# Performance work log

Hardware: AMD Instinct MI355X
Metric: run time of the kernel (lower is better)

The kernel has to match this reference:

```python
import jax, jax.numpy as jnp
import numpy as np

PAD = 1
K = 3  # kernel_size


def conv2d(x, w, b):
    y = jax.lax.conv_general_dilated(
        x, w, window_strides=(1, 1), padding=((PAD, PAD), (PAD, PAD)),
        dimension_numbers=("NCHW", "OIHW", "NCHW"))
    return y + b[None, :, None, None]


def deform_conv2d(x, offset, weight, bias):
    # torchvision.ops.deform_conv2d semantics (stride=1, dilation=1, 1 offset group)
    B, C, H, W = x.shape
    O = weight.shape[0]
    K2 = K * K
    off = offset.reshape(B, K2, 2, H, W)  # [...,0]=dy, [...,1]=dx
    ky, kx = jnp.meshgrid(jnp.arange(K), jnp.arange(K), indexing="ij")
    ky = ky.reshape(K2).astype(x.dtype)
    kx = kx.reshape(K2).astype(x.dtype)
    hh = jnp.arange(H, dtype=x.dtype)
    ww = jnp.arange(W, dtype=x.dtype)
    # sampling coords, shape [B, K2, H, W]
    py = off[:, :, 0] + ky[None, :, None, None] + hh[None, None, :, None] - PAD
    px = off[:, :, 1] + kx[None, :, None, None] + ww[None, None, None, :] - PAD

    y0 = jnp.floor(py)
    x0 = jnp.floor(px)
    wy = (py - y0)[:, None]  # [B,1,K2,H,W]
    wx = (px - x0)[:, None]

    xf = x.reshape(B, C, H * W)

    def gather(iy, ix):
        valid = (iy >= 0) & (iy < H) & (ix >= 0) & (ix < W)
        iyc = jnp.clip(iy, 0, H - 1).astype(jnp.int32)
        ixc = jnp.clip(ix, 0, W - 1).astype(jnp.int32)
        idx = (iyc * W + ixc).reshape(B, 1, K2 * H * W)
        v = jnp.take_along_axis(xf, idx, axis=2).reshape(B, C, K2, H, W)
        return v * valid.reshape(B, 1, K2, H, W).astype(x.dtype)

    v00 = gather(y0, x0)
    v01 = gather(y0, x0 + 1)
    v10 = gather(y0 + 1, x0)
    v11 = gather(y0 + 1, x0 + 1)
    sampled = (v00 * (1 - wy) * (1 - wx) + v01 * (1 - wy) * wx
               + v10 * wy * (1 - wx) + v11 * wy * wx)  # [B,C,K2,H,W]
    out = jnp.einsum("bckhw,ock->bohw", sampled, weight.reshape(O, C, K2))
    return out + bias[None, :, None, None]


def setup_inputs() -> dict:
    key = jax.random.key(0)
    k1, k2, k3, k4, k5 = jax.random.split(key, 5)
    B, C, H, W = 4, 64, 192, 192
    O = 64
    x = jax.random.normal(k1, (B, C, H, W), dtype=jnp.float32)
    w_off = jax.random.normal(k2, (2 * K * K, C, K, K), dtype=jnp.float32) * 0.05
    b_off = jnp.zeros((2 * K * K,), dtype=jnp.float32)
    w_conv = jax.random.normal(k3, (O, C, K, K), dtype=jnp.float32) * (1.0 / np.sqrt(C * K * K))
    b_conv = jax.random.normal(k4, (O,), dtype=jnp.float32) * 0.01
    return {"x": x, "w_off": w_off, "b_off": b_off, "w_conv": w_conv, "b_conv": b_conv}


def reference(x, w_off, b_off, w_conv, b_conv):
    offset = conv2d(x, w_off, b_off)
    y = deform_conv2d(x, offset, w_conv, b_conv)
    return conv2d(y, w_conv, b_conv)  # module reuses self.conv on deform output
```

## Files before the change

### kernel.cpp

```cpp
#include <hip/hip_runtime.h>

constexpr int B = 4;
constexpr int C = 64;
constexpr int O = 64;
constexpr int OOFF = 18;
constexpr int H = 192;
constexpr int W = 192;

typedef __attribute__((ext_vector_type(8))) short short8;
typedef __attribute__((ext_vector_type(4))) float float4v;
typedef __attribute__((ext_vector_type(2))) float f32x2;
typedef __attribute__((ext_vector_type(2))) uint u32x2;
typedef __attribute__((ext_vector_type(2))) __bf16 bf16x2;

__device__ inline ushort f2bf(float f) {
  return __builtin_bit_cast(ushort, (__bf16)f);
}
__device__ inline uint pk2bf(float lo, float hi) {
  bf16x2 v;
  v.x = (__bf16)lo;
  v.y = (__bf16)hi;
  return __builtin_bit_cast(uint, v);
}
__device__ inline f32x2 upk(uint u) {
  u32x2 t;
  t.x = u << 16;
  t.y = u & 0xffff0000u;
  return __builtin_bit_cast(f32x2, t);
}

__global__ __launch_bounds__(256) void k_pre(const float* __restrict__ x,
                                             ushort* __restrict__ xtb,
                                             const float* __restrict__ w_conv,
                                             ushort* __restrict__ wBf,
                                             const float* __restrict__ w_off,
                                             ushort* __restrict__ wOf) {
  __shared__ float tile[64][17];
  const int bid = blockIdx.x;
  const int tid = threadIdx.x;
  if (bid < 9216) {
    const int w0 = (bid % 12) * 16;
    const int h = (bid / 12) % 192;
    const int b = bid / 2304;
    const int wl = tid & 15;
    const int c0 = tid >> 4;
#pragma unroll
    for (int r = 0; r < 4; ++r) {
      const int c = c0 + r * 16;
      tile[c][wl] = x[(((size_t)b * C + c) * H + h) * W + w0 + wl];
    }
    __syncthreads();
    const int c = tid & 63;
    const int qq = tid >> 6;
#pragma unroll
    for (int r = 0; r < 4; ++r) {
      const int wq = qq + r * 4;
      xtb[(((size_t)b * H + h) * W + w0 + wq) * C + c] = f2bf(tile[c][wq]);
    }
  } else if (bid < 9360) {
    const int i = (bid - 9216) * 256 + tid;
    const int j = i & 7;
    const int lane = (i >> 3) & 63;
    const int nt = (i >> 9) & 3;
    const int kstep = (i >> 11) & 1;
    const int kk = i >> 12;
    const int n = nt + 4 * (lane & 15);
    const int c = kstep * 32 + ((lane >> 4) & 3) * 8 + j;
    wBf[i] = f2bf(w_conv[((size_t)n * C + c) * 9 + kk]);
  } else {
    const int i = (bid - 9360) * 256 + tid;
    const int j = i & 7;
    const int lane = (i >> 3) & 63;
    const int nt = (i >> 9) & 1;
    const int ks = (i >> 10) & 1;
    const int kk = i >> 11;
    const int n = nt * 16 + (lane & 15);
    const int c = ks * 32 + ((lane >> 4) & 3) * 8 + j;
    wOf[i] = (n < OOFF) ? f2bf(w_off[((size_t)n * C + c) * 9 + kk]) : (ushort)0;
  }
}

__global__ __launch_bounds__(128) void k_fused(
    const ushort* __restrict__ xtb, const ushort* __restrict__ wOf,
    const float* __restrict__ b_off, const ushort* __restrict__ wBf,
    const float* __restrict__ b_conv, ushort* __restrict__ yt) {
  __shared__ ushort sA[2][2][64][8];
  __shared__ __align__(16) float offBuf[2][16][20];

  const int bid = blockIdx.x;
  const int xcd = bid & 7;
  const int s0 = bid >> 3;
  const int b = xcd >> 1;
  const int half = xcd & 1;
  const int th = s0 / 24;
  const int tw = s0 % 24;

  const int tid = threadIdx.x;
  const int wave = tid >> 6, lane = tid & 63;
  const int h0 = half * 96 + th * 4 + wave * 2;
  const int w0 = tw * 8;

  const int col = lane & 15, quad = lane >> 4;
  const int p = lane >> 2, qtr = lane & 3;
  const int prow = p >> 3, pcol = p & 7;
  const int h = h0 + prow, w = w0 + pcol;

  {
    float4v oacc[2];
#pragma unroll
    for (int nt = 0; nt < 2; ++nt) oacc[nt] = (float4v){0.f, 0.f, 0.f, 0.f};

    short8 oafr[2][2];

    auto oload = [&](int kk, int pb) {
      const int ky = kk / 3, kx = kk % 3;
      const int hh = h0 + (col >> 3) + ky - 1;
      const int ww = w0 + (col & 7) + kx - 1;
      const bool ok = ((unsigned)hh < (unsigned)H) && ((unsigned)ww < (unsigned)W);
      const int hhc = min(max(hh, 0), H - 1);
      const int wwc = min(max(ww, 0), W - 1);
      const ushort* pa = xtb + (((size_t)b * H + hhc) * W + wwc) * C + quad * 8;
#pragma unroll
      for (int ks = 0; ks < 2; ++ks) {
        short8 v = (short8)0;
        if (ok) v = *(const short8*)(pa + ks * 32);
        oafr[pb][ks] = v;
      }
    };

    oload(0, 0);
#pragma unroll
    for (int kk = 0; kk < 9; ++kk) {
      const int pb = kk & 1;
      if (kk < 8) oload(kk + 1, pb ^ 1);
#pragma unroll
      for (int ks = 0; ks < 2; ++ks)
#pragma unroll
        for (int nt = 0; nt < 2; ++nt) {
          const short8 bw =
              *(const short8*)&wOf[((((size_t)kk * 2 + ks) * 2 + nt) * 64 + lane) * 8];
          oacc[nt] = __builtin_amdgcn_mfma_f32_16x16x32_bf16(oafr[pb][ks], bw, oacc[nt], 0, 0, 0);
        }
    }

#pragma unroll
    for (int nt = 0; nt < 2; ++nt) {
      const int oc = nt * 16 + col;
      if (oc < OOFF) {
        const float bias = b_off[oc];
#pragma unroll
        for (int r = 0; r < 4; ++r)
          offBuf[wave][quad * 4 + r][oc] = oacc[nt][r] + bias;
      }
    }
  }

  const ushort* xbase = xtb + (size_t)b * H * W * C;
  const uint qoff = (uint)qtr * 16u;
  const float hm1 = (float)(h - 1), wm1 = (float)(w - 1);

  uint offs[4];
  float4 awv;
  uint4 gA[4], gB[4];

  auto calc = [&](int kk) {
    const float2 ov = *(const float2*)&offBuf[wave][p][2 * kk];
    const int ky = kk / 3, kx = kk % 3;
    const float pyf = ov.x + hm1 + (float)ky;
    const float pxf = ov.y + wm1 + (float)kx;
    const float fy0 = floorf(pyf), fx0 = floorf(pxf);
    const float wy = pyf - fy0, wx = pxf - fx0;
    const int iy0 = (int)fy0, ix0 = (int)fx0;
    const int iy1 = iy0 + 1, ix1 = ix0 + 1;
    const bool vy0 = (unsigned)iy0 < (unsigned)H;
    const bool vy1 = (unsigned)iy1 < (unsigned)H;
    const bool vx0 = (unsigned)ix0 < (unsigned)W;
    const bool vx1 = (unsigned)ix1 < (unsigned)W;
    awv.x = (vy0 && vx0) ? (1.f - wy) * (1.f - wx) : 0.f;
    awv.y = (vy0 && vx1) ? (1.f - wy) * wx : 0.f;
    awv.z = (vy1 && vx0) ? wy * (1.f - wx) : 0.f;
    awv.w = (vy1 && vx1) ? wy * wx : 0.f;
    const int cy0 = min(max(iy0, 0), H - 1), cy1 = min(max(iy1, 0), H - 1);
    const int cx0 = min(max(ix0, 0), W - 1), cx1 = min(max(ix1, 0), W - 1);
    offs[0] = (uint)((cy0 * W + cx0) * (C * 2)) + qoff;
    offs[1] = (uint)((cy0 * W + cx1) * (C * 2)) + qoff;
    offs[2] = (uint)((cy1 * W + cx0) * (C * 2)) + qoff;
    offs[3] = (uint)((cy1 * W + cx1) * (C * 2)) + qoff;
  };

  auto loadAB = [&]() {
#pragma unroll
    for (int c = 0; c < 4; ++c)
      gA[c] = *(const uint4*)((const char*)xbase + offs[c]);
#pragma unroll
    for (int c = 0; c < 4; ++c)
      gB[c] = *(const uint4*)((const char*)xbase + offs[c] + 64u);
  };
  auto blend = [&](const uint4* g, uint* pk) {
    const f32x2 a00 = {awv.x, awv.x};
    const f32x2 a01 = {awv.y, awv.y};
    const f32x2 a10 = {awv.z, awv.z};
    const f32x2 a11 = {awv.w, awv.w};
#pragma unroll
    for (int i = 0; i < 4; ++i) {
      f32x2 sv = upk(g[0][i]) * a00 + upk(g[1][i]) * a01 + upk(g[2][i]) * a10 + upk(g[3][i]) * a11;
      pk[i] = pk2bf(sv.x, sv.y);
    }
  };

  float4v acc[4];
#pragma unroll
  for (int nt = 0; nt < 4; ++nt) acc[nt] = (float4v){0.f, 0.f, 0.f, 0.f};

  calc(0);
  loadAB();
#pragma unroll
  for (int kk = 0; kk < 9; ++kk) {
    uint pkA[4];
    blend(gA, pkA);
    *(uint4*)&sA[wave][0][p | (qtr << 4)][0] = *(const uint4*)pkA;
    uint pkB[4];
    blend(gB, pkB);
    *(uint4*)&sA[wave][1][p | (qtr << 4)][0] = *(const uint4*)pkB;

    if (kk < 8) {
      calc(kk + 1);
      loadAB();
    }

#pragma unroll
    for (int ks = 0; ks < 2; ++ks) {
      const short8 a = *(const short8*)&sA[wave][ks][lane][0];
#pragma unroll
      for (int nt = 0; nt < 4; ++nt) {
        const short8 bb = *(const short8*)&wBf[((((size_t)kk * 2 + ks) * 4 + nt) * 64 + lane) * 8];
        acc[nt] = __builtin_amdgcn_mfma_f32_16x16x32_bf16(a, bb, acc[nt], 0, 0, 0);
      }
    }
  }

  float bias[4];
#pragma unroll
  for (int nt = 0; nt < 4; ++nt) bias[nt] = b_conv[4 * col + nt];
#pragma unroll
  for (int r = 0; r < 4; ++r) {
    const int pp = quad * 4 + r;
    const int hrow = h0 + (pp >> 3), wcol = w0 + (pp & 7);
    uint2 u;
    u.x = pk2bf(acc[0][r] + bias[0], acc[1][r] + bias[1]);
    u.y = pk2bf(acc[2][r] + bias[2], acc[3][r] + bias[3]);
    *(uint2*)&yt[((size_t)(b * H + hrow) * W + wcol) * C + 4 * col] = u;
  }
}

__global__ __launch_bounds__(256) void k_conv_main_mfma(
    const ushort* __restrict__ yt, const ushort* __restrict__ wBf,
    const float* __restrict__ b_conv, float* __restrict__ out) {
  const int w0 = blockIdx.x * 16;
  const int b = blockIdx.z;
  const int tid = threadIdx.x;
  const int wave = tid >> 6, lane = tid & 63;
  const int col = lane & 15, quad = lane >> 4;
  const int h0 = blockIdx.y * 8 + wave * 2;

  float4v acc[2][4];
#pragma unroll
  for (int mt = 0; mt < 2; ++mt)
#pragma unroll
    for (int nt = 0; nt < 4; ++nt) acc[mt][nt] = (float4v){0.f, 0.f, 0.f, 0.f};

  short8 bfr[2][2][4];
  short8 afr[2][2][2];

  auto load = [&](int kk, int pb) {
    const int ky = kk / 3, kx = kk % 3;
    const int ww = w0 + col + kx - 1;
    const bool wok = (unsigned)ww < (unsigned)W;
    const int wwc = min(max(ww, 0), W - 1);
#pragma unroll
    for (int ks = 0; ks < 2; ++ks)
#pragma unroll
      for (int nt = 0; nt < 4; ++nt)
        bfr[pb][ks][nt] = *(const short8*)&wBf[((((size_t)kk * 2 + ks) * 4 + nt) * 64 + lane) * 8];
#pragma unroll
    for (int mt = 0; mt < 2; ++mt) {
      const int hh = h0 + mt + ky - 1;
      const bool ok = wok && ((unsigned)hh < (unsigned)H);
      const int hhc = min(max(hh, 0), H - 1);
      const ushort* pa = yt + (((size_t)b * H + hhc) * W + wwc) * C + quad * 8;
#pragma unroll
      for (int ks = 0; ks < 2; ++ks) {
        short8 v = (short8)0;
        if (ok) v = *(const short8*)(pa + ks * 32);
        afr[pb][mt][ks] = v;
      }
    }
  };

  load(0, 0);
#pragma unroll
  for (int kk = 0; kk < 9; ++kk) {
    const int pb = kk & 1;
    if (kk < 8) load(kk + 1, pb ^ 1);
#pragma unroll
    for (int ks = 0; ks < 2; ++ks)
#pragma unroll
      for (int mt = 0; mt < 2; ++mt)
#pragma unroll
        for (int nt = 0; nt < 4; ++nt)
          acc[mt][nt] = __builtin_amdgcn_mfma_f32_16x16x32_bf16(afr[pb][mt][ks], bfr[pb][ks][nt],
                                                                acc[mt][nt], 0, 0, 0);
  }

  float bias[4];
#pragma unroll
  for (int nt = 0; nt < 4; ++nt) bias[nt] = b_conv[4 * col + nt];
#pragma unroll
  for (int mt = 0; mt < 2; ++mt) {
    const int h = h0 + mt;
#pragma unroll
    for (int nt = 0; nt < 4; ++nt) {
      const int oc = 4 * col + nt;
      float4 v;
      v.x = acc[mt][nt][0] + bias[nt];
      v.y = acc[mt][nt][1] + bias[nt];
      v.z = acc[mt][nt][2] + bias[nt];
      v.w = acc[mt][nt][3] + bias[nt];
      *(float4*)&out[(((size_t)b * O + oc) * H + h) * W + w0 + quad * 4] = v;
    }
  }
}

extern "C" void kernel_launch(void* const* d_in, const int* in_sizes, int n_in,
                              void* d_out, int out_size, void* d_ws, size_t ws_size,
                              hipStream_t stream) {
  const float* x = (const float*)d_in[0];
  const float* w_off = (const float*)d_in[1];
  const float* b_off = (const float*)d_in[2];
  const float* w_conv = (const float*)d_in[3];
  const float* b_conv = (const float*)d_in[4];
  float* out = (float*)d_out;

  ushort* xtb = (ushort*)d_ws;
  ushort* yt = xtb + (size_t)B * H * W * C;
  ushort* wBf = yt + (size_t)B * H * W * C;
  ushort* wOf = wBf + 36864;

  k_pre<<<dim3(9432), dim3(256), 0, stream>>>(x, xtb, w_conv, wBf, w_off, wOf);
  k_fused<<<dim3(4608), dim3(128), 0, stream>>>(xtb, wOf, b_off, wBf, b_conv, yt);
  k_conv_main_mfma<<<dim3(W / 16, H / 8, B), dim3(256), 0, stream>>>(yt, wBf, b_conv, out);
}
```

Measured before the change: 200.1 us.

## Enlarge per-wave pixel tiles to reuse weight fragments across four M-tiles

The fused offset/deform kernel now gives each single-wave block an 8x8 pixel tile (four 16-pixel M-tiles) instead of 2x8 per wave. Each weight fragment loaded from global memory is reused across four MFMAs, and the deform loop is restructured to pipeline gather/blend across M-tiles. The final conv kernel likewise doubles rows per wave to four and loads B fragments inline, shared across four M-tiles. The aim is to cut redundant weight loads; the cost is more registers and fewer blocks, and the reduced unrolling may add loop overhead.

Result: slower. 218.1 us (+9.0%).

```diff
diff --git a/kernel.cpp b/kernel.cpp
--- a/kernel.cpp
+++ b/kernel.cpp
@@ -80,12 +80,12 @@
   }
 }
 
-__global__ __launch_bounds__(128) void k_fused(
+__global__ __launch_bounds__(64) void k_fused(
     const ushort* __restrict__ xtb, const ushort* __restrict__ wOf,
     const float* __restrict__ b_off, const ushort* __restrict__ wBf,
     const float* __restrict__ b_conv, ushort* __restrict__ yt) {
-  __shared__ ushort sA[2][2][64][8];
-  __shared__ __align__(16) float offBuf[2][16][20];
+  __shared__ ushort sA[2][64][8];
+  __shared__ __align__(16) float offBuf[64][20];
 
   const int bid = blockIdx.x;
   const int xcd = bid & 7;
@@ -94,42 +94,43 @@
   const int half = xcd & 1;
   const int th = s0 / 24;
   const int tw = s0 % 24;
-
-  const int tid = threadIdx.x;
-  const int wave = tid >> 6, lane = tid & 63;
-  const int h0 = half * 96 + th * 4 + wave * 2;
-  const int w0 = tw * 8;
-
+  const int h0 = half * 96 + th * 8, w0 = tw * 8;
+
+  const int lane = threadIdx.x;
   const int col = lane & 15, quad = lane >> 4;
-  const int p = lane >> 2, qtr = lane & 3;
-  const int prow = p >> 3, pcol = p & 7;
-  const int h = h0 + prow, w = w0 + pcol;
+  const int pq = lane >> 2, qtr = lane & 3;
 
   {
-    float4v oacc[2];
-#pragma unroll
-    for (int nt = 0; nt < 2; ++nt) oacc[nt] = (float4v){0.f, 0.f, 0.f, 0.f};
-
-    short8 oafr[2][2];
+    float4v oacc[4][2];
+#pragma unroll
+    for (int mt = 0; mt < 4; ++mt)
+#pragma unroll
+      for (int nt = 0; nt < 2; ++nt) oacc[mt][nt] = (float4v){0.f, 0.f, 0.f, 0.f};
+
+    short8 oafr[2][4][2];
 
     auto oload = [&](int kk, int pb) {
       const int ky = kk / 3, kx = kk % 3;
-      const int hh = h0 + (col >> 3) + ky - 1;
       const int ww = w0 + (col & 7) + kx - 1;
-      const bool ok = ((unsigned)hh < (unsigned)H) && ((unsigned)ww < (unsigned)W);
-      const int hhc = min(max(hh, 0), H - 1);
+      const bool wok = (unsigned)ww < (unsigned)W;
       const int wwc = min(max(ww, 0), W - 1);
-      const ushort* pa = xtb + (((size_t)b * H + hhc) * W + wwc) * C + quad * 8;
-#pragma unroll
-      for (int ks = 0; ks < 2; ++ks) {
-        short8 v = (short8)0;
-        if (ok) v = *(const short8*)(pa + ks * 32);
-        oafr[pb][ks] = v;
+#pragma unroll
+      for (int mt = 0; mt < 4; ++mt) {
+        const int hh = h0 + 2 * mt + (col >> 3) + ky - 1;
+        const bool ok = wok && ((unsigned)hh < (unsigned)H);
+        const int hhc = min(max(hh, 0), H - 1);
+        const ushort* pa = xtb + (((size_t)b * H + hhc) * W + wwc) * C + quad * 8;
+#pragma unroll
+        for (int ks = 0; ks < 2; ++ks) {
+          short8 v = (short8)0;
+          if (ok) v = *(const short8*)(pa + ks * 32);
+          oafr[pb][mt][ks] = v;
+        }
       }
     };
 
     oload(0, 0);
-#pragma unroll
+#pragma unroll 2
     for (int kk = 0; kk < 9; ++kk) {
       const int pb = kk & 1;
       if (kk < 8) oload(kk + 1, pb ^ 1);
@@ -139,7 +140,10 @@
         for (int nt = 0; nt < 2; ++nt) {
           const short8 bw =
               *(const short8*)&wOf[((((size_t)kk * 2 + ks) * 2 + nt) * 64 + lane) * 8];
-          oacc[nt] = __builtin_amdgcn_mfma_f32_16x16x32_bf16(oafr[pb][ks], bw, oacc[nt], 0, 0, 0);
+#pragma unroll
+          for (int mt = 0; mt < 4; ++mt)
+            oacc[mt][nt] =
+                __builtin_amdgcn_mfma_f32_16x16x32_bf16(oafr[pb][mt][ks], bw, oacc[mt][nt], 0, 0, 0);
         }
     }
 
@@ -149,25 +153,27 @@
       if (oc < OOFF) {
         const float bias = b_off[oc];
 #pragma unroll
-        for (int r = 0; r < 4; ++r)
-          offBuf[wave][quad * 4 + r][oc] = oacc[nt][r] + bias;
+        for (int mt = 0; mt < 4; ++mt)
+#pragma unroll
+          for (int r = 0; r < 4; ++r)
+            offBuf[mt * 16 + quad * 4 + r][oc] = oacc[mt][nt][r] + bias;
       }
     }
   }
 
   const ushort* xbase = xtb + (size_t)b * H * W * C;
   const uint qoff = (uint)qtr * 16u;
-  const float hm1 = (float)(h - 1), wm1 = (float)(w - 1);
 
   uint offs[4];
   float4 awv;
   uint4 gA[4], gB[4];
-
-  auto calc = [&](int kk) {
-    const float2 ov = *(const float2*)&offBuf[wave][p][2 * kk];
+  short8 bb[2][4];
+
+  auto calc = [&](int kk, int pp) {
+    const float2 ov = *(const float2*)&offBuf[pp][2 * kk];
     const int ky = kk / 3, kx = kk % 3;
-    const float pyf = ov.x + hm1 + (float)ky;
-    const float pxf = ov.y + wm1 + (float)kx;
+    const float pyf = ov.x + (float)(h0 + (pp >> 3) + ky - 1);
+    const float pxf = ov.y + (float)(w0 + (pp & 7) + kx - 1);
     const float fy0 = floorf(pyf), fx0 = floorf(pxf);
     const float wy = pyf - fy0, wx = pxf - fx0;
     const int iy0 = (int)fy0, ix0 = (int)fx0;
@@ -208,33 +214,44 @@
     }
   };
 
-  float4v acc[4];
-#pragma unroll
-  for (int nt = 0; nt < 4; ++nt) acc[nt] = (float4v){0.f, 0.f, 0.f, 0.f};
-
-  calc(0);
+  float4v acc[4][4];
+#pragma unroll
+  for (int mt = 0; mt < 4; ++mt)
+#pragma unroll
+    for (int nt = 0; nt < 4; ++nt) acc[mt][nt] = (float4v){0.f, 0.f, 0.f, 0.f};
+
+  calc(0, 0 * 16 + pq);
   loadAB();
-#pragma unroll
+#pragma unroll 1
   for (int kk = 0; kk < 9; ++kk) {
-    uint pkA[4];
-    blend(gA, pkA);
-    *(uint4*)&sA[wave][0][p | (qtr << 4)][0] = *(const uint4*)pkA;
-    uint pkB[4];
-    blend(gB, pkB);
-    *(uint4*)&sA[wave][1][p | (qtr << 4)][0] = *(const uint4*)pkB;
-
-    if (kk < 8) {
-      calc(kk + 1);
-      loadAB();
-    }
-
-#pragma unroll
-    for (int ks = 0; ks < 2; ++ks) {
-      const short8 a = *(const short8*)&sA[wave][ks][lane][0];
-#pragma unroll
-      for (int nt = 0; nt < 4; ++nt) {
-        const short8 bb = *(const short8*)&wBf[((((size_t)kk * 2 + ks) * 4 + nt) * 64 + lane) * 8];
-        acc[nt] = __builtin_amdgcn_mfma_f32_16x16x32_bf16(a, bb, acc[nt], 0, 0, 0);
+#pragma unroll
+    for (int ks = 0; ks < 2; ++ks)
+#pragma unroll
+      for (int nt = 0; nt < 4; ++nt)
+        bb[ks][nt] = *(const short8*)&wBf[((((size_t)kk * 2 + ks) * 4 + nt) * 64 + lane) * 8];
+
+#pragma unroll
+    for (int mt = 0; mt < 4; ++mt) {
+      uint pkA[4];
+      blend(gA, pkA);
+      *(uint4*)&sA[0][pq | (qtr << 4)][0] = *(const uint4*)pkA;
+      uint pkB[4];
+      blend(gB, pkB);
+      *(uint4*)&sA[1][pq | (qtr << 4)][0] = *(const uint4*)pkB;
+
+      {
+        const int nmt = (mt + 1) & 3;
+        const int nkk = (mt == 3) ? min(kk + 1, 8) : kk;
+        calc(nkk, nmt * 16 + pq);
+        loadAB();
+      }
+
+#pragma unroll
+      for (int ks = 0; ks < 2; ++ks) {
+        const short8 a = *(const short8*)&sA[ks][lane][0];
+#pragma unroll
+        for (int nt = 0; nt < 4; ++nt)
+          acc[mt][nt] = __builtin_amdgcn_mfma_f32_16x16x32_bf16(a, bb[ks][nt], acc[mt][nt], 0, 0, 0);
       }
     }
   }
@@ -243,14 +260,16 @@
 #pragma unroll
   for (int nt = 0; nt < 4; ++nt) bias[nt] = b_conv[4 * col + nt];
 #pragma unroll
-  for (int r = 0; r < 4; ++r) {
-    const int pp = quad * 4 + r;
-    const int hrow = h0 + (pp >> 3), wcol = w0 + (pp & 7);
-    uint2 u;
-    u.x = pk2bf(acc[0][r] + bias[0], acc[1][r] + bias[1]);
-    u.y = pk2bf(acc[2][r] + bias[2], acc[3][r] + bias[3]);
-    *(uint2*)&yt[((size_t)(b * H + hrow) * W + wcol) * C + 4 * col] = u;
-  }
+  for (int mt = 0; mt < 4; ++mt)
+#pragma unroll
+    for (int r = 0; r < 4; ++r) {
+      const int pp = mt * 16 + quad * 4 + r;
+      const int hrow = h0 + (pp >> 3), wcol = w0 + (pp & 7);
+      uint2 u;
+      u.x = pk2bf(acc[mt][0][r] + bias[0], acc[mt][1][r] + bias[1]);
+      u.y = pk2bf(acc[mt][2][r] + bias[2], acc[mt][3][r] + bias[3]);
+      *(uint2*)&yt[((size_t)(b * H + hrow) * W + wcol) * C + 4 * col] = u;
+    }
 }
 
 __global__ __launch_bounds__(256) void k_conv_main_mfma(
@@ -261,16 +280,15 @@
   const int tid = threadIdx.x;
   const int wave = tid >> 6, lane = tid & 63;
   const int col = lane & 15, quad = lane >> 4;
-  const int h0 = blockIdx.y * 8 + wave * 2;
-
-  float4v acc[2][4];
-#pragma unroll
-  for (int mt = 0; mt < 2; ++mt)
+  const int h0 = blockIdx.y * 16 + wave * 4;
+
+  float4v acc[4][4];
+#pragma unroll
+  for (int mt = 0; mt < 4; ++mt)
 #pragma unroll
     for (int nt = 0; nt < 4; ++nt) acc[mt][nt] = (float4v){0.f, 0.f, 0.f, 0.f};
 
-  short8 bfr[2][2][4];
-  short8 afr[2][2][2];
+  short8 afr[2][4][2];
 
   auto load = [&](int kk, int pb) {
     const int ky = kk / 3, kx = kk % 3;
@@ -278,12 +296,7 @@
     const bool wok = (unsigned)ww < (unsigned)W;
     const int wwc = min(max(ww, 0), W - 1);
 #pragma unroll
-    for (int ks = 0; ks < 2; ++ks)
-#pragma unroll
-      for (int nt = 0; nt < 4; ++nt)
-        bfr[pb][ks][nt] = *(const short8*)&wBf[((((size_t)kk * 2 + ks) * 4 + nt) * 64 + lane) * 8];
-#pragma unroll
-    for (int mt = 0; mt < 2; ++mt) {
+    for (int mt = 0; mt < 4; ++mt) {
       const int hh = h0 + mt + ky - 1;
       const bool ok = wok && ((unsigned)hh < (unsigned)H);
       const int hhc = min(max(hh, 0), H - 1);
@@ -298,25 +311,27 @@
   };
 
   load(0, 0);
-#pragma unroll
+#pragma unroll 2
   for (int kk = 0; kk < 9; ++kk) {
     const int pb = kk & 1;
     if (kk < 8) load(kk + 1, pb ^ 1);
 #pragma unroll
     for (int ks = 0; ks < 2; ++ks)
 #pragma unroll
-      for (int mt = 0; mt < 2; ++mt)
-#pragma unroll
-        for (int nt = 0; nt < 4; ++nt)
-          acc[mt][nt] = __builtin_amdgcn_mfma_f32_16x16x32_bf16(afr[pb][mt][ks], bfr[pb][ks][nt],
-                                                                acc[mt][nt], 0, 0, 0);
+      for (int nt = 0; nt < 4; ++nt) {
+        const short8 bb = *(const short8*)&wBf[((((size_t)kk * 2 + ks) * 4 + nt) * 64 + lane) * 8];
+#pragma unroll
+        for (int mt = 0; mt < 4; ++mt)
+          acc[mt][nt] =
+              __builtin_amdgcn_mfma_f32_16x16x32_bf16(afr[pb][mt][ks], bb, acc[mt][nt], 0, 0, 0);
+      }
   }
 
   float bias[4];
 #pragma unroll
   for (int nt = 0; nt < 4; ++nt) bias[nt] = b_conv[4 * col + nt];
 #pragma unroll
-  for (int mt = 0; mt < 2; ++mt) {
+  for (int mt = 0; mt < 4; ++mt) {
     const int h = h0 + mt;
 #pragma unroll
     for (int nt = 0; nt < 4; ++nt) {
@@ -347,6 +362,6 @@
   ushort* wOf = wBf + 36864;
 
   k_pre<<<dim3(9432), dim3(256), 0, stream>>>(x, xtb, w_conv, wBf, w_off, wOf);
-  k_fused<<<dim3(4608), dim3(128), 0, stream>>>(xtb, wOf, b_off, wBf, b_conv, yt);
-  k_conv_main_mfma<<<dim3(W / 16, H / 8, B), dim3(256), 0, stream>>>(yt, wBf, b_conv, out);
-}
+  k_fused<<<dim3(2304), dim3(64), 0, stream>>>(xtb, wOf, b_off, wBf, b_conv, yt);
+  k_conv_main_mfma<<<dim3(W / 16, H / 16, B), dim3(256), 0, stream>>>(yt, wBf, b_conv, out);
+}
```

## Stage input halo tile in LDS for deformable bilinear gathers

Applied to the files above, without the earlier changes.

The fused deform kernel now uses 256-thread blocks covering an 8x8 output tile and first loads a swizzled 20x24-pixel, 64-channel bf16 halo of the input into shared memory. Bilinear samples that fall inside the halo are read from LDS, and samples outside it fall back to global loads. This cuts scattered global/L2 gathers but adds about 61KB of LDS per block, which limits occupancy. It also drops the software prefetch of the next tap's samples and preloads weight fragments per tap with a non-unrolled loop.

Result: slower. 206.5 us (+3.2%).

```diff
diff --git a/kernel.cpp b/kernel.cpp
--- a/kernel.cpp
+++ b/kernel.cpp
@@ -80,12 +80,13 @@
   }
 }
 
-__global__ __launch_bounds__(128) void k_fused(
+__global__ __launch_bounds__(256) void k_fused(
     const ushort* __restrict__ xtb, const ushort* __restrict__ wOf,
     const float* __restrict__ b_off, const ushort* __restrict__ wBf,
     const float* __restrict__ b_conv, ushort* __restrict__ yt) {
-  __shared__ ushort sA[2][2][64][8];
-  __shared__ __align__(16) float offBuf[2][16][20];
+  __shared__ __align__(16) ushort stg[20 * 24 * 64];
+  __shared__ ushort sA[4][2][64][8];
+  __shared__ __align__(16) float offBuf[4][16][20];
 
   const int bid = blockIdx.x;
   const int xcd = bid & 7;
@@ -94,16 +95,23 @@
   const int half = xcd & 1;
   const int th = s0 / 24;
   const int tw = s0 % 24;
+  const int h0 = half * 96 + th * 8, w0 = tw * 8;
 
   const int tid = threadIdx.x;
   const int wave = tid >> 6, lane = tid & 63;
-  const int h0 = half * 96 + th * 4 + wave * 2;
-  const int w0 = tw * 8;
-
+  const int hb = h0 + wave * 2;
   const int col = lane & 15, quad = lane >> 4;
   const int p = lane >> 2, qtr = lane & 3;
-  const int prow = p >> 3, pcol = p & 7;
-  const int h = h0 + prow, w = w0 + pcol;
+
+  for (int i = wave; i < 60; i += 4) {
+    const int r = i / 3, c3 = i % 3;
+    const int ry = min(max(h0 - 6 + r, 0), H - 1);
+    const int cxs = w0 - 8 + c3 * 8 + (lane >> 3);
+    const int cx = min(max(cxs, 0), W - 1);
+    const uint4 v = *(const uint4*)(xtb + (((size_t)b * H + ry) * W + cx) * C + (lane & 7) * 8);
+    const int dst = r * 1536 + (c3 * 8 + (lane >> 3)) * 64 + (((lane & 7) ^ ((lane >> 3) & 7)) * 8);
+    *(uint4*)&stg[dst] = v;
+  }
 
   {
     float4v oacc[2];
@@ -114,7 +122,7 @@
 
     auto oload = [&](int kk, int pb) {
       const int ky = kk / 3, kx = kk % 3;
-      const int hh = h0 + (col >> 3) + ky - 1;
+      const int hh = hb + (col >> 3) + ky - 1;
       const int ww = w0 + (col & 7) + kx - 1;
       const bool ok = ((unsigned)hh < (unsigned)H) && ((unsigned)ww < (unsigned)W);
       const int hhc = min(max(hh, 0), H - 1);
@@ -129,7 +137,7 @@
     };
 
     oload(0, 0);
-#pragma unroll
+#pragma unroll 2
     for (int kk = 0; kk < 9; ++kk) {
       const int pb = kk & 1;
       if (kk < 8) oload(kk + 1, pb ^ 1);
@@ -155,19 +163,41 @@
     }
   }
 
+  __syncthreads();
+
   const ushort* xbase = xtb + (size_t)b * H * W * C;
-  const uint qoff = (uint)qtr * 16u;
-  const float hm1 = (float)(h - 1), wm1 = (float)(w - 1);
-
-  uint offs[4];
-  float4 awv;
-  uint4 gA[4], gB[4];
-
-  auto calc = [&](int kk) {
+  const uint q16 = (uint)qtr * 16u;
+
+  auto blend = [&](const uint4* g, const float4& aw, uint* pk) {
+    const f32x2 a00 = {aw.x, aw.x};
+    const f32x2 a01 = {aw.y, aw.y};
+    const f32x2 a10 = {aw.z, aw.z};
+    const f32x2 a11 = {aw.w, aw.w};
+#pragma unroll
+    for (int i = 0; i < 4; ++i) {
+      f32x2 sv = upk(g[0][i]) * a00 + upk(g[1][i]) * a01 + upk(g[2][i]) * a10 + upk(g[3][i]) * a11;
+      pk[i] = pk2bf(sv.x, sv.y);
+    }
+  };
+
+  float4v acc[4];
+#pragma unroll
+  for (int nt = 0; nt < 4; ++nt) acc[nt] = (float4v){0.f, 0.f, 0.f, 0.f};
+
+#pragma unroll 1
+  for (int kk = 0; kk < 9; ++kk) {
+    short8 bb[2][4];
+#pragma unroll
+    for (int ks = 0; ks < 2; ++ks)
+#pragma unroll
+      for (int nt = 0; nt < 4; ++nt)
+        bb[ks][nt] = *(const short8*)&wBf[((((size_t)kk * 2 + ks) * 4 + nt) * 64 + lane) * 8];
+
+    const int ky = kk / 3, kx = kk % 3;
+
     const float2 ov = *(const float2*)&offBuf[wave][p][2 * kk];
-    const int ky = kk / 3, kx = kk % 3;
-    const float pyf = ov.x + hm1 + (float)ky;
-    const float pxf = ov.y + wm1 + (float)kx;
+    const float pyf = ov.x + (float)(hb + (p >> 3) + ky - 1);
+    const float pxf = ov.y + (float)(w0 + (p & 7) + kx - 1);
     const float fy0 = floorf(pyf), fx0 = floorf(pxf);
     const float wy = pyf - fy0, wx = pxf - fx0;
     const int iy0 = (int)fy0, ix0 = (int)fx0;
@@ -176,66 +206,60 @@
     const bool vy1 = (unsigned)iy1 < (unsigned)H;
     const bool vx0 = (unsigned)ix0 < (unsigned)W;
     const bool vx1 = (unsigned)ix1 < (unsigned)W;
+    float4 awv;
     awv.x = (vy0 && vx0) ? (1.f - wy) * (1.f - wx) : 0.f;
     awv.y = (vy0 && vx1) ? (1.f - wy) * wx : 0.f;
     awv.z = (vy1 && vx0) ? wy * (1.f - wx) : 0.f;
     awv.w = (vy1 && vx1) ? wy * wx : 0.f;
     const int cy0 = min(max(iy0, 0), H - 1), cy1 = min(max(iy1, 0), H - 1);
     const int cx0 = min(max(ix0, 0), W - 1), cx1 = min(max(ix1, 0), W - 1);
-    offs[0] = (uint)((cy0 * W + cx0) * (C * 2)) + qoff;
-    offs[1] = (uint)((cy0 * W + cx1) * (C * 2)) + qoff;
-    offs[2] = (uint)((cy1 * W + cx0) * (C * 2)) + qoff;
-    offs[3] = (uint)((cy1 * W + cx1) * (C * 2)) + qoff;
-  };
-
-  auto loadAB = [&]() {
-#pragma unroll
-    for (int c = 0; c < 4; ++c)
-      gA[c] = *(const uint4*)((const char*)xbase + offs[c]);
-#pragma unroll
-    for (int c = 0; c < 4; ++c)
-      gB[c] = *(const uint4*)((const char*)xbase + offs[c] + 64u);
-  };
-  auto blend = [&](const uint4* g, uint* pk) {
-    const f32x2 a00 = {awv.x, awv.x};
-    const f32x2 a01 = {awv.y, awv.y};
-    const f32x2 a10 = {awv.z, awv.z};
-    const f32x2 a11 = {awv.w, awv.w};
-#pragma unroll
-    for (int i = 0; i < 4; ++i) {
-      f32x2 sv = upk(g[0][i]) * a00 + upk(g[1][i]) * a01 + upk(g[2][i]) * a10 + upk(g[3][i]) * a11;
-      pk[i] = pk2bf(sv.x, sv.y);
-    }
-  };
-
-  float4v acc[4];
-#pragma unroll
-  for (int nt = 0; nt < 4; ++nt) acc[nt] = (float4v){0.f, 0.f, 0.f, 0.f};
-
-  calc(0);
-  loadAB();
-#pragma unroll
-  for (int kk = 0; kk < 9; ++kk) {
+
+    uint4 gA[4], gB[4];
+    const int sy0 = cy0 - h0 + 6, sy1 = cy1 - h0 + 6;
+    const int sx0 = cx0 - w0 + 8, sx1 = cx1 - w0 + 8;
+    if (((unsigned)sy0 <= 19u) & ((unsigned)sy1 <= 19u) & ((unsigned)sx0 <= 23u) &
+        ((unsigned)sx1 <= 23u)) {
+      const int cA0 = sx0 * 64 + ((qtr ^ (sx0 & 7)) * 8);
+      const int cA1 = sx1 * 64 + ((qtr ^ (sx1 & 7)) * 8);
+      const int r0 = sy0 * 1536, r1 = sy1 * 1536;
+      const int a00 = r0 + cA0, a01 = r0 + cA1, a10 = r1 + cA0, a11 = r1 + cA1;
+      gA[0] = *(const uint4*)&stg[a00];
+      gB[0] = *(const uint4*)&stg[a00 ^ 32];
+      gA[1] = *(const uint4*)&stg[a01];
+      gB[1] = *(const uint4*)&stg[a01 ^ 32];
+      gA[2] = *(const uint4*)&stg[a10];
+      gB[2] = *(const uint4*)&stg[a10 ^ 32];
+      gA[3] = *(const uint4*)&stg[a11];
+      gB[3] = *(const uint4*)&stg[a11 ^ 32];
+    } else {
+      const char* xb = (const char*)xbase;
+      const uint o00 = (uint)((cy0 * W + cx0) * (C * 2)) + q16;
+      const uint o01 = (uint)((cy0 * W + cx1) * (C * 2)) + q16;
+      const uint o10 = (uint)((cy1 * W + cx0) * (C * 2)) + q16;
+      const uint o11 = (uint)((cy1 * W + cx1) * (C * 2)) + q16;
+      gA[0] = *(const uint4*)(xb + o00);
+      gB[0] = *(const uint4*)(xb + o00 + 64u);
+      gA[1] = *(const uint4*)(xb + o01);
+      gB[1] = *(const uint4*)(xb + o01 + 64u);
+      gA[2] = *(const uint4*)(xb + o10);
+      gB[2] = *(const uint4*)(xb + o10 + 64u);
+      gA[3] = *(const uint4*)(xb + o11);
+      gB[3] = *(const uint4*)(xb + o11 + 64u);
+    }
+
     uint pkA[4];
-    blend(gA, pkA);
+    blend(gA, awv, pkA);
     *(uint4*)&sA[wave][0][p | (qtr << 4)][0] = *(const uint4*)pkA;
     uint pkB[4];
-    blend(gB, pkB);
+    blend(gB, awv, pkB);
     *(uint4*)&sA[wave][1][p | (qtr << 4)][0] = *(const uint4*)pkB;
-
-    if (kk < 8) {
-      calc(kk + 1);
-      loadAB();
-    }
 
 #pragma unroll
     for (int ks = 0; ks < 2; ++ks) {
       const short8 a = *(const short8*)&sA[wave][ks][lane][0];
 #pragma unroll
-      for (int nt = 0; nt < 4; ++nt) {
-        const short8 bb = *(const short8*)&wBf[((((size_t)kk * 2 + ks) * 4 + nt) * 64 + lane) * 8];
-        acc[nt] = __builtin_amdgcn_mfma_f32_16x16x32_bf16(a, bb, acc[nt], 0, 0, 0);
-      }
+      for (int nt = 0; nt < 4; ++nt)
+        acc[nt] = __builtin_amdgcn_mfma_f32_16x16x32_bf16(a, bb[ks][nt], acc[nt], 0, 0, 0);
     }
   }
 
@@ -245,7 +269,7 @@
 #pragma unroll
   for (int r = 0; r < 4; ++r) {
     const int pp = quad * 4 + r;
-    const int hrow = h0 + (pp >> 3), wcol = w0 + (pp & 7);
+    const int hrow = hb + (pp >> 3), wcol = w0 + (pp & 7);
     uint2 u;
     u.x = pk2bf(acc[0][r] + bias[0], acc[1][r] + bias[1]);
     u.y = pk2bf(acc[2][r] + bias[2], acc[3][r] + bias[3]);
@@ -347,6 +371,6 @@
   ushort* wOf = wBf + 36864;
 
   k_pre<<<dim3(9432), dim3(256), 0, stream>>>(x, xtb, w_conv, wBf, w_off, wOf);
-  k_fused<<<dim3(4608), dim3(128), 0, stream>>>(xtb, wOf, b_off, wBf, b_conv, yt);
+  k_fused<<<dim3(2304), dim3(256), 0, stream>>>(xtb, wOf, b_off, wBf, b_conv, yt);
   k_conv_main_mfma<<<dim3(W / 16, H / 8, B), dim3(256), 0, stream>>>(yt, wBf, b_conv, out);
 }
```

## Build MFMA A-fragments in registers and enlarge fused deform-conv blocks to four waves

Applied to the files above, without the earlier changes.

The fused offset/deform kernel now has each lane sample the pixel and channel group that matches its MFMA A-operand slot directly. The blended bf16 values feed the MFMA without a round trip through shared memory, which removes the sA buffer and its LDS traffic. Blocks grow from two to four waves (8x8 pixel tiles, half the grid) and all weight fragments for a tap are loaded before the blend. This raises register pressure, and the offset-conv loop is only partially unrolled to compensate.

Measured after the change: 246.4 us. +23.1%, slower.

```diff
diff --git a/kernel.cpp b/kernel.cpp
--- a/kernel.cpp
+++ b/kernel.cpp
@@ -80,30 +80,25 @@
   }
 }
 
-__global__ __launch_bounds__(128) void k_fused(
+__global__ __launch_bounds__(256) void k_fused(
     const ushort* __restrict__ xtb, const ushort* __restrict__ wOf,
     const float* __restrict__ b_off, const ushort* __restrict__ wBf,
     const float* __restrict__ b_conv, ushort* __restrict__ yt) {
-  __shared__ ushort sA[2][2][64][8];
-  __shared__ __align__(16) float offBuf[2][16][20];
+  __shared__ __align__(16) float offBuf[4][16][20];
 
   const int bid = blockIdx.x;
   const int xcd = bid & 7;
   const int s0 = bid >> 3;
   const int b = xcd >> 1;
   const int half = xcd & 1;
-  const int th = s0 / 24;
+  const int th = half * 12 + s0 / 24;
   const int tw = s0 % 24;
+  const int h0 = th * 8, w0 = tw * 8;
 
   const int tid = threadIdx.x;
   const int wave = tid >> 6, lane = tid & 63;
-  const int h0 = half * 96 + th * 4 + wave * 2;
-  const int w0 = tw * 8;
-
+  const int hb = h0 + wave * 2;
   const int col = lane & 15, quad = lane >> 4;
-  const int p = lane >> 2, qtr = lane & 3;
-  const int prow = p >> 3, pcol = p & 7;
-  const int h = h0 + prow, w = w0 + pcol;
 
   {
     float4v oacc[2];
@@ -114,7 +109,7 @@
 
     auto oload = [&](int kk, int pb) {
       const int ky = kk / 3, kx = kk % 3;
-      const int hh = h0 + (col >> 3) + ky - 1;
+      const int hh = hb + (col >> 3) + ky - 1;
       const int ww = w0 + (col & 7) + kx - 1;
       const bool ok = ((unsigned)hh < (unsigned)H) && ((unsigned)ww < (unsigned)W);
       const int hhc = min(max(hh, 0), H - 1);
@@ -129,7 +124,7 @@
     };
 
     oload(0, 0);
-#pragma unroll
+#pragma unroll 2
     for (int kk = 0; kk < 9; ++kk) {
       const int pb = kk & 1;
       if (kk < 8) oload(kk + 1, pb ^ 1);
@@ -156,18 +151,18 @@
   }
 
   const ushort* xbase = xtb + (size_t)b * H * W * C;
-  const uint qoff = (uint)qtr * 16u;
-  const float hm1 = (float)(h - 1), wm1 = (float)(w - 1);
+  const uint qoff = (uint)quad * 16u;
+  const int ph = hb + (col >> 3), pw = w0 + (col & 7);
 
   uint offs[4];
   float4 awv;
   uint4 gA[4], gB[4];
 
   auto calc = [&](int kk) {
-    const float2 ov = *(const float2*)&offBuf[wave][p][2 * kk];
+    const float2 ov = *(const float2*)&offBuf[wave][col][2 * kk];
     const int ky = kk / 3, kx = kk % 3;
-    const float pyf = ov.x + hm1 + (float)ky;
-    const float pxf = ov.y + wm1 + (float)kx;
+    const float pyf = ov.x + (float)(ph + ky - 1);
+    const float pxf = ov.y + (float)(pw + kx - 1);
     const float fy0 = floorf(pyf), fx0 = floorf(pxf);
     const float wy = pyf - fy0, wx = pxf - fx0;
     const int iy0 = (int)fy0, ix0 = (int)fx0;
@@ -216,27 +211,30 @@
   loadAB();
 #pragma unroll
   for (int kk = 0; kk < 9; ++kk) {
-    uint pkA[4];
+    short8 bb[2][4];
+#pragma unroll
+    for (int ks = 0; ks < 2; ++ks)
+#pragma unroll
+      for (int nt = 0; nt < 4; ++nt)
+        bb[ks][nt] = *(const short8*)&wBf[((((size_t)kk * 2 + ks) * 4 + nt) * 64 + lane) * 8];
+
+    uint pkA[4], pkB[4];
     blend(gA, pkA);
-    *(uint4*)&sA[wave][0][p | (qtr << 4)][0] = *(const uint4*)pkA;
-    uint pkB[4];
     blend(gB, pkB);
-    *(uint4*)&sA[wave][1][p | (qtr << 4)][0] = *(const uint4*)pkB;
 
     if (kk < 8) {
       calc(kk + 1);
       loadAB();
     }
 
-#pragma unroll
-    for (int ks = 0; ks < 2; ++ks) {
-      const short8 a = *(const short8*)&sA[wave][ks][lane][0];
-#pragma unroll
-      for (int nt = 0; nt < 4; ++nt) {
-        const short8 bb = *(const short8*)&wBf[((((size_t)kk * 2 + ks) * 4 + nt) * 64 + lane) * 8];
-        acc[nt] = __builtin_amdgcn_mfma_f32_16x16x32_bf16(a, bb, acc[nt], 0, 0, 0);
-      }
-    }
+    const short8 aA = *(const short8*)&pkA[0];
+    const short8 aB = *(const short8*)&pkB[0];
+#pragma unroll
+    for (int nt = 0; nt < 4; ++nt)
+      acc[nt] = __builtin_amdgcn_mfma_f32_16x16x32_bf16(aA, bb[0][nt], acc[nt], 0, 0, 0);
+#pragma unroll
+    for (int nt = 0; nt < 4; ++nt)
+      acc[nt] = __builtin_amdgcn_mfma_f32_16x16x32_bf16(aB, bb[1][nt], acc[nt], 0, 0, 0);
   }
 
   float bias[4];
@@ -245,7 +243,7 @@
 #pragma unroll
   for (int r = 0; r < 4; ++r) {
     const int pp = quad * 4 + r;
-    const int hrow = h0 + (pp >> 3), wcol = w0 + (pp & 7);
+    const int hrow = hb + (pp >> 3), wcol = w0 + (pp & 7);
     uint2 u;
     u.x = pk2bf(acc[0][r] + bias[0], acc[1][r] + bias[1]);
     u.y = pk2bf(acc[2][r] + bias[2], acc[3][r] + bias[3]);
@@ -347,6 +345,6 @@
   ushort* wOf = wBf + 36864;
 
   k_pre<<<dim3(9432), dim3(256), 0, stream>>>(x, xtb, w_conv, wBf, w_off, wOf);
-  k_fused<<<dim3(4608), dim3(128), 0, stream>>>(xtb, wOf, b_off, wBf, b_conv, yt);
+  k_fused<<<dim3(2304), dim3(256), 0, stream>>>(xtb, wOf, b_off, wBf, b_conv, yt);
   k_conv_main_mfma<<<dim3(W / 16, H / 8, B), dim3(256), 0, stream>>>(yt, wBf, b_conv, out);
 }
```
